# Kernel tuning notes

Hardware: AMD Instinct MI355X
Metric: run time of the kernel (lower is better)

Reference implementation:

```python
import jax, jax.numpy as jnp
import numpy as np

C = 256      # in_channels
NH = 4       # n_heads
NG = 32      # GroupNorm num_groups
EPS = 1e-5   # torch GroupNorm default eps


def _conv1x1(x, w, b):
    # 1x1 conv == per-pixel channel matmul. x: (B,C,H,W), w: (O,C), b: (O,)
    return jnp.einsum('oc,bchw->bohw', w, x) + b[None, :, None, None]


def _groupnorm(x, gamma, beta):
    b, c, h, w = x.shape
    xg = x.reshape(b, NG, c // NG, h, w)
    mu = xg.mean(axis=(2, 3, 4), keepdims=True)
    var = xg.var(axis=(2, 3, 4), keepdims=True)
    xn = ((xg - mu) * jax.lax.rsqrt(var + EPS)).reshape(b, c, h, w)
    return xn * gamma[None, :, None, None] + beta[None, :, None, None]


def setup_inputs() -> dict:
    key = jax.random.key(0)
    ks = jax.random.split(key, 5)
    B, H, W = 2, 64, 64
    s = 1.0 / np.sqrt(C).astype(np.float32)
    return {
        'x': jax.random.normal(ks[0], (B, C, H, W), jnp.float32),
        'gamma': jnp.ones((C,), jnp.float32),
        'beta': jnp.zeros((C,), jnp.float32),
        'wq': jax.random.normal(ks[1], (C, C), jnp.float32) * s,
        'bq': jnp.zeros((C,), jnp.float32),
        'wk': jax.random.normal(ks[2], (C, C), jnp.float32) * s,
        'bk': jnp.zeros((C,), jnp.float32),
        'wv': jax.random.normal(ks[3], (C, C), jnp.float32) * s,
        'bv': jnp.zeros((C,), jnp.float32),
        'wp': jax.random.normal(ks[4], (C, C), jnp.float32) * s,
        'bp': jnp.zeros((C,), jnp.float32),
    }


def reference(x, gamma, beta, wq, bq, wk, bk, wv, bv, wp, bp):
    b, c, h, w = x.shape
    c_ = c // NH  # head dim
    hn = _groupnorm(x, gamma, beta)
    # NOTE: original splits channels as (head_dim, n_heads) with head_dim leading
    q = _conv1x1(hn, wq, bq).reshape(b, c_, NH, h * w)
    k = _conv1x1(hn, wk, bk).reshape(b, c_, NH, h * w)
    v = _conv1x1(hn, wv, bv).reshape(b, c_, NH, h * w)
    scores = jnp.einsum('bcnq,bcnk->bqkn', q, k) * (c_ ** -0.5)  # (B,S,S,NH)
    attn = jax.nn.softmax(scores, axis=2)  # softmax over key axis
    out = jnp.einsum('bcnd,bqdn->bcnq', v, attn).reshape(b, c, h, w)
    return x + _conv1x1(out, wp, bp)
```

## Files before the change

### kernel.cpp

```cpp
#include <hip/hip_runtime.h>

#define CH 256
#define NHEAD 4
#define HD 64
#define SP 4096
#define NB 2
#define QSCALE 0.1803368801111204f

typedef __attribute__((ext_vector_type(8))) short bf16x8;
typedef __attribute__((ext_vector_type(4))) float f32x4;
typedef unsigned int u32;
typedef unsigned short u16;

__device__ inline u16 b16(float f) {
    u32 u = __float_as_uint(f);
    return (u16)((u + 0x8000u) >> 16);
}
__device__ inline float fexp2(float x) { return __builtin_amdgcn_exp2f(x); }

__global__ __launch_bounds__(256) void prep_kernel(
    const float* __restrict__ x, float2* __restrict__ part,
    const float* __restrict__ wq, const float* __restrict__ wk,
    const float* __restrict__ wv, const float* __restrict__ wp,
    u16* __restrict__ wqb, u16* __restrict__ wkb,
    u16* __restrict__ wvb, u16* __restrict__ wpb)
{
    int tid = threadIdx.x;
    if (blockIdx.x < 256) {
        int bgq = blockIdx.x;
        int bg = bgq >> 2, qtr = bgq & 3;
        const float4* xp = (const float4*)(x + (size_t)bg * 8 * SP) + qtr * 2048;
        float s = 0.f, ss = 0.f;
        for (int i = tid; i < 2048; i += 256) {
            float4 u = xp[i];
            s  += (u.x + u.y) + (u.z + u.w);
            ss += (u.x * u.x + u.y * u.y) + (u.z * u.z + u.w * u.w);
        }
#pragma unroll
        for (int off = 32; off > 0; off >>= 1) {
            s  += __shfl_down(s, off);
            ss += __shfl_down(ss, off);
        }
        __shared__ float ws_s[4], ws_q[4];
        int w = tid >> 6;
        if ((tid & 63) == 0) { ws_s[w] = s; ws_q[w] = ss; }
        __syncthreads();
        if (tid == 0)
            part[bgq] = make_float2(ws_s[0] + ws_s[1] + ws_s[2] + ws_s[3],
                                    ws_q[0] + ws_q[1] + ws_q[2] + ws_q[3]);
    } else {
        int idx = (blockIdx.x - 256) * 256 + tid;
        int m = idx >> 16, i = idx & 65535;
        if (m == 0)      wqb[i] = b16(wq[i] * QSCALE);
        else if (m == 1) wkb[i] = b16(wk[i]);
        else if (m == 2) wvb[i] = b16(wv[i]);
        else {
            int c = i >> 8, chan = i & 255;
            int n = chan >> 6, d = chan & 63;
            wpb[i] = b16(wp[c * 256 + d * 4 + n]);
        }
    }
}

__global__ __launch_bounds__(256) void qkv_gemm_kernel(
    const float* __restrict__ x, const float2* __restrict__ part,
    const float* __restrict__ gamma, const float* __restrict__ beta,
    const u16* __restrict__ wqb, const u16* __restrict__ wkb,
    const u16* __restrict__ wvb,
    const float* __restrict__ bq, const float* __restrict__ bk,
    const float* __restrict__ bv,
    u16* __restrict__ qt, u16* __restrict__ ktp, u16* __restrict__ vtp)
{
    int zz = blockIdx.y;
    int b = zz / 3, p = zz % 3;
    const u16* W = (p == 0) ? wqb : (p == 1) ? wkb : wvb;
    const float* bias = (p == 0) ? bq : (p == 1) ? bk : bv;
    float bs = (p == 0) ? QSCALE : 1.f;
    int s0 = blockIdx.x * 32;
    int tid = threadIdx.x, w = tid >> 6, lane = tid & 63;
    int t = lane >> 4, ln = lane & 15;

    __shared__ u16 SB[10240];
    __shared__ float As[256], Bs[256];

    {
        int c = tid, bg = b * 32 + (c >> 3);
        float s = 0.f, ss = 0.f;
#pragma unroll
        for (int q = 0; q < 4; q++) { float2 pp = part[bg * 4 + q]; s += pp.x; ss += pp.y; }
        float mu = s * (1.f / 32768.f);
        float var = ss * (1.f / 32768.f) - mu * mu;
        float rs = rsqrtf(var + 1e-5f);
        float ga = gamma[c];
        As[c] = rs * ga;
        Bs[c] = beta[c] - mu * rs * ga;
    }
    __syncthreads();

    {
        int cb = tid >> 3;
        int sseg = (tid & 7) * 4;
#pragma unroll
        for (int it = 0; it < 8; it++) {
            int c = it * 32 + cb;
            float4 v = *(const float4*)&x[((size_t)b * CH + c) * SP + s0 + sseg];
            float aa = As[c], bb = Bs[c];
            SB[(sseg + 0) * 264 + c] = b16(fmaf(aa, v.x, bb));
            SB[(sseg + 1) * 264 + c] = b16(fmaf(aa, v.y, bb));
            SB[(sseg + 2) * 264 + c] = b16(fmaf(aa, v.z, bb));
            SB[(sseg + 3) * 264 + c] = b16(fmaf(aa, v.w, bb));
        }
    }
    __syncthreads();

    f32x4 acc[4][2];
#pragma unroll
    for (int og = 0; og < 4; og++)
#pragma unroll
        for (int sg = 0; sg < 2; sg++)
            acc[og][sg] = (f32x4){0.f, 0.f, 0.f, 0.f};

#pragma unroll
    for (int ks = 0; ks < 8; ks++) {
        bf16x8 af[4], bfv[2];
#pragma unroll
        for (int og = 0; og < 4; og++)
            af[og] = *(const bf16x8*)&W[(size_t)(w * 64 + og * 16 + ln) * CH + ks * 32 + t * 8];
#pragma unroll
        for (int sg = 0; sg < 2; sg++)
            bfv[sg] = *(const bf16x8*)&SB[(sg * 16 + ln) * 264 + ks * 32 + t * 8];
#pragma unroll
        for (int og = 0; og < 4; og++)
#pragma unroll
            for (int sg = 0; sg < 2; sg++)
                acc[og][sg] = __builtin_amdgcn_mfma_f32_16x16x32_bf16(
                    af[og], bfv[sg], acc[og][sg], 0, 0, 0);
    }
    __syncthreads();

    if (p < 2) {
#pragma unroll
        for (int og = 0; og < 4; og++)
#pragma unroll
            for (int sg = 0; sg < 2; sg++)
#pragma unroll
                for (int r = 0; r < 4; r++) {
                    int o = w * 64 + og * 16 + 4 * t + r;
                    SB[(r * 32 + sg * 16 + ln) * 72 + (w * 16 + og * 4 + t)] =
                        b16(acc[og][sg][r] + bias[o] * bs);
                }
        __syncthreads();
        if (p == 0) {
#pragma unroll
            for (int it = 0; it < 4; it++) {
                int idx = it * 256 + tid;
                int o8 = idx & 7, sl = (idx >> 3) & 31, n = idx >> 8;
                *(uint4*)&qt[((size_t)(b * 4 + n) * SP + s0 + sl) * HD + o8 * 8] =
                    *(const uint4*)&SB[(n * 32 + sl) * 72 + o8 * 8];
            }
        } else {
#pragma unroll
            for (int it = 0; it < 4; it++) {
                int idx = it * 256 + tid;
                int o8 = idx & 7, sl = (idx >> 3) & 31, n = idx >> 8;
                int key = s0 + sl;
                int g = ((key >> 4) & 3) * 2 + (o8 >> 2);
                int lp = (key & 15) + 16 * (o8 & 3);
                *(uint4*)&ktp[(size_t)(b * 4 + n) * SP * HD +
                              (size_t)(key >> 6) * 4096 + g * 512 + lp * 8] =
                    *(const uint4*)&SB[(n * 32 + sl) * 72 + o8 * 8];
            }
        }
    } else {
#pragma unroll
        for (int og = 0; og < 4; og++)
#pragma unroll
            for (int sg = 0; sg < 2; sg++)
#pragma unroll
                for (int r = 0; r < 4; r++) {
                    int o = w * 64 + og * 16 + 4 * t + r;
                    SB[(r * 64 + w * 16 + og * 4 + t) * 40 + sg * 16 + ln] =
                        b16(acc[og][sg][r] + bias[o]);
                }
        __syncthreads();
#pragma unroll
        for (int it = 0; it < 4; it++) {
            int idx = it * 256 + tid;
            int so8 = idx & 3, d = (idx >> 2) & 63, n = idx >> 8;
            int key = s0 + so8 * 8;
            int g = ((d >> 4) & 3) * 2 + ((key >> 5) & 1);
            int lp = (d & 15) + 16 * ((key >> 3) & 3);
            *(uint4*)&vtp[(size_t)(b * 4 + n) * SP * HD +
                          (size_t)(key >> 6) * 4096 + g * 512 + lp * 8] =
                *(const uint4*)&SB[(n * 64 + d) * 40 + so8 * 8];
        }
    }
}

__global__ __launch_bounds__(256, 3) void attn_kernel(
    const u16* __restrict__ qtb, const u16* __restrict__ ktp,
    const u16* __restrict__ vtp, u16* __restrict__ opart,
    float* __restrict__ lpart)
{
    int bx = blockIdx.x;
    int z = bx & 7, qt_i = (bx >> 3) & 31, sp = bx >> 8;
    int sq0 = qt_i * 128;
    int tile0 = sp * 16;
    const u16* qz = qtb + (size_t)z * SP * HD;
    const u16* kz = ktp + (size_t)z * SP * HD;
    const u16* vz = vtp + (size_t)z * SP * HD;

    int tid = threadIdx.x, w = tid >> 6, l = tid & 63;
    int t = l >> 4, ln = l & 15;

    __shared__ __align__(16) u32 Pb[4][2][512];

    bf16x8 qf[2][2];
#pragma unroll
    for (int qg = 0; qg < 2; qg++)
#pragma unroll
        for (int ds = 0; ds < 2; ds++)
            qf[qg][ds] = *(const bf16x8*)&qz[
                (size_t)(sq0 + w * 32 + qg * 16 + ln) * HD + ds * 32 + t * 8];

    bf16x8 kf[8], vf[8];
#pragma unroll
    for (int g = 0; g < 8; g++)
        kf[g] = *(const bf16x8*)&kz[(size_t)tile0 * 4096 + g * 512 + l * 8];

    float lsum[2] = {0.f, 0.f};
    f32x4 oacc[2][4];
#pragma unroll
    for (int qg = 0; qg < 2; qg++)
#pragma unroll
        for (int dg = 0; dg < 4; dg++)
            oacc[qg][dg] = (f32x4){0.f, 0.f, 0.f, 0.f};

    const f32x4 z4 = {0.f, 0.f, 0.f, 0.f};
    f32x4 sa[2][4];

    auto ep = [&](int qg) {
#pragma unroll
        for (int kg = 0; kg < 4; kg++) {
            float e0 = fexp2(sa[qg][kg][0]);
            float e1 = fexp2(sa[qg][kg][1]);
            float e2 = fexp2(sa[qg][kg][2]);
            float e3 = fexp2(sa[qg][kg][3]);
            lsum[qg] += (e0 + e1) + (e2 + e3);
            u32 p0 = __builtin_amdgcn_perm(__float_as_uint(e1), __float_as_uint(e0), 0x07060302u);
            u32 p1 = __builtin_amdgcn_perm(__float_as_uint(e3), __float_as_uint(e2), 0x07060302u);
            int Lt = ln + 16 * (2 * (kg & 1) + (t >> 1));
            int ksg = kg >> 1;
            *(uint2*)&Pb[w][qg][(ksg * 64 + Lt) * 4 + 2 * (t & 1)] =
                make_uint2(p0, p1);
        }
    };

    for (int kti = 0; kti < 16; kti++) {
        size_t tb = (size_t)(tile0 + kti) * 4096;

#pragma unroll
        for (int g = 0; g < 8; g++)
            vf[g] = *(const bf16x8*)&vz[tb + g * 512 + l * 8];

#pragma unroll
        for (int kg = 0; kg < 4; kg++) {
#pragma unroll
            for (int qg = 0; qg < 2; qg++)
                sa[qg][kg] = __builtin_amdgcn_mfma_f32_16x16x32_bf16(
                    kf[kg * 2 + 0], qf[qg][0], z4, 0, 0, 0);
        }
#pragma unroll
        for (int kg = 0; kg < 4; kg++) {
#pragma unroll
            for (int qg = 0; qg < 2; qg++)
                sa[qg][kg] = __builtin_amdgcn_mfma_f32_16x16x32_bf16(
                    kf[kg * 2 + 1], qf[qg][1], sa[qg][kg], 0, 0, 0);
        }

        if (kti < 15) {
            size_t nb = tb + 4096;
#pragma unroll
            for (int g = 0; g < 8; g++)
                kf[g] = *(const bf16x8*)&kz[nb + g * 512 + l * 8];
        }

        ep(0);
#pragma unroll
        for (int qg = 0; qg < 2; qg++) {
            if (qg == 0) ep(1);
            bf16x8 pf[2];
#pragma unroll
            for (int ksg = 0; ksg < 2; ksg++)
                pf[ksg] = *(const bf16x8*)&Pb[w][qg][(ksg * 64 + l) * 4];
#pragma unroll
            for (int ksg = 0; ksg < 2; ksg++)
#pragma unroll
                for (int dg = 0; dg < 4; dg++)
                    oacc[qg][dg] = __builtin_amdgcn_mfma_f32_16x16x32_bf16(
                        pf[ksg], vf[dg * 2 + ksg], oacc[qg][dg], 0, 0, 0);
        }
    }

#pragma unroll
    for (int qg = 0; qg < 2; qg++) {
        lsum[qg] += __shfl_xor(lsum[qg], 16);
        lsum[qg] += __shfl_xor(lsum[qg], 32);
    }

    size_t obase = (size_t)(sp * 8 + z) * SP;
    u16* po = (u16*)&Pb[w][0][0];
#pragma unroll
    for (int qg = 0; qg < 2; qg++)
#pragma unroll
        for (int dg = 0; dg < 4; dg++)
#pragma unroll
            for (int r = 0; r < 4; r++)
                po[(qg * 16 + 4 * t + r) * 64 + dg * 16 + ln] = b16(oacc[qg][dg][r]);
#pragma unroll
    for (int i = 0; i < 4; i++) {
        int f = i * 512 + l * 8;
        int qloc = f >> 6, d0 = f & 63;
        uint4 v = *(const uint4*)&po[f];
        *(uint4*)&opart[(obase + sq0 + w * 32 + qloc) * HD + d0] = v;
    }
    if (t == 0)
#pragma unroll
        for (int qg = 0; qg < 2; qg++)
            lpart[obase + sq0 + w * 32 + qg * 16 + ln] = lsum[qg];
}

__global__ __launch_bounds__(256) void proj_gemm_kernel(
    const u16* __restrict__ opart, const float* __restrict__ lpart,
    const u16* __restrict__ wpb, const float* __restrict__ bp,
    const float* __restrict__ x, float* __restrict__ out)
{
    int b = blockIdx.y;
    int s0 = blockIdx.x * 16;
    int tid = threadIdx.x, w = tid >> 6, lane = tid & 63;
    int t = lane >> 4, ln = lane & 15;

    float linv[4];
#pragma unroll
    for (int n = 0; n < 4; n++) {
        float s = 0.f;
#pragma unroll
        for (int sp = 0; sp < 4; sp++)
            s += lpart[(size_t)(sp * 8 + b * 4 + n) * SP + s0 + ln];
        linv[n] = 1.f / s;
    }

    f32x4 acc[4];
#pragma unroll
    for (int og = 0; og < 4; og++)
        acc[og] = (f32x4){0.f, 0.f, 0.f, 0.f};

#pragma unroll
    for (int ks = 0; ks < 8; ks++) {
        bf16x8 af[4];
#pragma unroll
        for (int og = 0; og < 4; og++)
            af[og] = *(const bf16x8*)&wpb[(size_t)(w * 64 + og * 16 + ln) * CH + ks * 32 + t * 8];

        int n = ks >> 1;
        int d0 = (ks & 1) * 32 + t * 8;
        u32 ov[4][4];
#pragma unroll
        for (int sp = 0; sp < 4; sp++) {
            uint4 o4 = *(const uint4*)&opart[
                ((size_t)(sp * 8 + b * 4 + n) * SP + s0 + ln) * HD + d0];
            ov[sp][0] = o4.x; ov[sp][1] = o4.y; ov[sp][2] = o4.z; ov[sp][3] = o4.w;
        }
        float inv = linv[n];
        union { u32 u[4]; bf16x8 v; } bu;
#pragma unroll
        for (int i = 0; i < 4; i++) {
            float lo = 0.f, hi = 0.f;
#pragma unroll
            for (int sp = 0; sp < 4; sp++) {
                lo += __uint_as_float(ov[sp][i] << 16);
                hi += __uint_as_float(ov[sp][i] & 0xffff0000u);
            }
            u16 rl = b16(lo * inv), rh = b16(hi * inv);
            bu.u[i] = ((u32)rh << 16) | rl;
        }
#pragma unroll
        for (int og = 0; og < 4; og++)
            acc[og] = __builtin_amdgcn_mfma_f32_16x16x32_bf16(
                af[og], bu.v, acc[og], 0, 0, 0);
    }

#pragma unroll
    for (int og = 0; og < 4; og++)
#pragma unroll
        for (int r = 0; r < 4; r++) {
            int c = w * 64 + og * 16 + 4 * t + r;
            size_t idx = ((size_t)b * CH + c) * SP + s0 + ln;
            out[idx] = acc[og][r] + bp[c] + x[idx];
        }
}

extern "C" void kernel_launch(void* const* d_in, const int* in_sizes, int n_in,
                              void* d_out, int out_size, void* d_ws, size_t ws_size,
                              hipStream_t stream)
{
    const float* x     = (const float*)d_in[0];
    const float* gamma = (const float*)d_in[1];
    const float* beta  = (const float*)d_in[2];
    const float* wq = (const float*)d_in[3]; const float* bq = (const float*)d_in[4];
    const float* wk = (const float*)d_in[5]; const float* bk = (const float*)d_in[6];
    const float* wv = (const float*)d_in[7]; const float* bv = (const float*)d_in[8];
    const float* wp = (const float*)d_in[9]; const float* bp = (const float*)d_in[10];
    float* out = (float*)d_out;

    const size_t TEN = (size_t)8 * SP * HD;
    char* wsb = (char*)d_ws;
    float2* part = (float2*)wsb;
    u16* wqb = (u16*)(wsb + 4096);
    u16* wkb = wqb + 65536;
    u16* wvb = wkb + 65536;
    u16* wpb = wvb + 65536;
    u16* qt  = wpb + 65536;
    u16* ktp = qt + TEN;
    u16* vtp = ktp + TEN;
    u16* opart = vtp + TEN;
    float* lpart = (float*)(opart + 4 * TEN);

    prep_kernel<<<dim3(1280), dim3(256), 0, stream>>>(
        x, part, wq, wk, wv, wp, wqb, wkb, wvb, wpb);
    qkv_gemm_kernel<<<dim3(128, 6), dim3(256), 0, stream>>>(
        x, part, gamma, beta, wqb, wkb, wvb, bq, bk, bv, qt, ktp, vtp);
    attn_kernel<<<dim3(1024), dim3(256), 0, stream>>>(qt, ktp, vtp, opart, lpart);
    proj_gemm_kernel<<<dim3(256, 2), dim3(256), 0, stream>>>(
        opart, lpart, wpb, bp, x, out);
}
```

Measured before the change: 159.8 us.

## Increase split-KV parallelism, shrink QKV tiles, and stage merged attention output in LDS

The attention kernel now takes the KV split count as a runtime parameter and uses 8 splits when the workspace is large enough, otherwise 4. Launch bounds are raised to 5 waves per SIMD to favour occupancy. The QKV GEMM uses 16-pixel tiles, doubling its grid and cutting LDS use. The projection kernel merges the split partials once into a shared-memory tile instead of reloading them inside each k-step. More splits add partial-output traffic and merge work, and the higher occupancy target may force register spills in the attention kernel.

```diff
diff --git a/kernel.cpp b/kernel.cpp
--- a/kernel.cpp
+++ b/kernel.cpp
@@ -76,11 +76,11 @@
     const u16* W = (p == 0) ? wqb : (p == 1) ? wkb : wvb;
     const float* bias = (p == 0) ? bq : (p == 1) ? bk : bv;
     float bs = (p == 0) ? QSCALE : 1.f;
-    int s0 = blockIdx.x * 32;
+    int s0 = blockIdx.x * 16;
     int tid = threadIdx.x, w = tid >> 6, lane = tid & 63;
     int t = lane >> 4, ln = lane & 15;
 
-    __shared__ u16 SB[10240];
+    __shared__ u16 SB[6144];
     __shared__ float As[256], Bs[256];
 
     {
@@ -98,11 +98,10 @@
     __syncthreads();
 
     {
-        int cb = tid >> 3;
-        int sseg = (tid & 7) * 4;
-#pragma unroll
-        for (int it = 0; it < 8; it++) {
-            int c = it * 32 + cb;
+        int cb = tid >> 2, sseg = (tid & 3) * 4;
+#pragma unroll
+        for (int it = 0; it < 4; it++) {
+            int c = it * 64 + cb;
             float4 v = *(const float4*)&x[((size_t)b * CH + c) * SP + s0 + sseg];
             float aa = As[c], bb = Bs[c];
             SB[(sseg + 0) * 264 + c] = b16(fmaf(aa, v.x, bb));
@@ -113,28 +112,22 @@
     }
     __syncthreads();
 
-    f32x4 acc[4][2];
+    f32x4 acc[4];
 #pragma unroll
     for (int og = 0; og < 4; og++)
-#pragma unroll
-        for (int sg = 0; sg < 2; sg++)
-            acc[og][sg] = (f32x4){0.f, 0.f, 0.f, 0.f};
+        acc[og] = (f32x4){0.f, 0.f, 0.f, 0.f};
 
 #pragma unroll
     for (int ks = 0; ks < 8; ks++) {
-        bf16x8 af[4], bfv[2];
+        bf16x8 af[4];
 #pragma unroll
         for (int og = 0; og < 4; og++)
             af[og] = *(const bf16x8*)&W[(size_t)(w * 64 + og * 16 + ln) * CH + ks * 32 + t * 8];
-#pragma unroll
-        for (int sg = 0; sg < 2; sg++)
-            bfv[sg] = *(const bf16x8*)&SB[(sg * 16 + ln) * 264 + ks * 32 + t * 8];
-#pragma unroll
-        for (int og = 0; og < 4; og++)
-#pragma unroll
-            for (int sg = 0; sg < 2; sg++)
-                acc[og][sg] = __builtin_amdgcn_mfma_f32_16x16x32_bf16(
-                    af[og], bfv[sg], acc[og][sg], 0, 0, 0);
+        bf16x8 bfv = *(const bf16x8*)&SB[ln * 264 + ks * 32 + t * 8];
+#pragma unroll
+        for (int og = 0; og < 4; og++)
+            acc[og] = __builtin_amdgcn_mfma_f32_16x16x32_bf16(
+                af[og], bfv, acc[og], 0, 0, 0);
     }
     __syncthreads();
 
@@ -142,70 +135,66 @@
 #pragma unroll
         for (int og = 0; og < 4; og++)
 #pragma unroll
-            for (int sg = 0; sg < 2; sg++)
-#pragma unroll
-                for (int r = 0; r < 4; r++) {
-                    int o = w * 64 + og * 16 + 4 * t + r;
-                    SB[(r * 32 + sg * 16 + ln) * 72 + (w * 16 + og * 4 + t)] =
-                        b16(acc[og][sg][r] + bias[o] * bs);
-                }
+            for (int r = 0; r < 4; r++) {
+                int o = w * 64 + og * 16 + 4 * t + r;
+                SB[(r * 16 + ln) * 72 + (w * 16 + og * 4 + t)] =
+                    b16(acc[og][r] + bias[o] * bs);
+            }
         __syncthreads();
         if (p == 0) {
 #pragma unroll
-            for (int it = 0; it < 4; it++) {
-                int idx = it * 256 + tid;
-                int o8 = idx & 7, sl = (idx >> 3) & 31, n = idx >> 8;
+            for (int it = 0; it < 2; it++) {
+                int f = it * 256 + tid;
+                int o8 = f & 7, sl = (f >> 3) & 15, n = f >> 7;
                 *(uint4*)&qt[((size_t)(b * 4 + n) * SP + s0 + sl) * HD + o8 * 8] =
-                    *(const uint4*)&SB[(n * 32 + sl) * 72 + o8 * 8];
+                    *(const uint4*)&SB[(n * 16 + sl) * 72 + o8 * 8];
             }
         } else {
 #pragma unroll
-            for (int it = 0; it < 4; it++) {
-                int idx = it * 256 + tid;
-                int o8 = idx & 7, sl = (idx >> 3) & 31, n = idx >> 8;
+            for (int it = 0; it < 2; it++) {
+                int f = it * 256 + tid;
+                int o8 = f & 7, sl = (f >> 3) & 15, n = f >> 7;
                 int key = s0 + sl;
                 int g = ((key >> 4) & 3) * 2 + (o8 >> 2);
                 int lp = (key & 15) + 16 * (o8 & 3);
                 *(uint4*)&ktp[(size_t)(b * 4 + n) * SP * HD +
                               (size_t)(key >> 6) * 4096 + g * 512 + lp * 8] =
-                    *(const uint4*)&SB[(n * 32 + sl) * 72 + o8 * 8];
+                    *(const uint4*)&SB[(n * 16 + sl) * 72 + o8 * 8];
             }
         }
     } else {
 #pragma unroll
         for (int og = 0; og < 4; og++)
 #pragma unroll
-            for (int sg = 0; sg < 2; sg++)
-#pragma unroll
-                for (int r = 0; r < 4; r++) {
-                    int o = w * 64 + og * 16 + 4 * t + r;
-                    SB[(r * 64 + w * 16 + og * 4 + t) * 40 + sg * 16 + ln] =
-                        b16(acc[og][sg][r] + bias[o]);
-                }
+            for (int r = 0; r < 4; r++) {
+                int o = w * 64 + og * 16 + 4 * t + r;
+                SB[(r * 64 + w * 16 + og * 4 + t) * 24 + ln] =
+                    b16(acc[og][r] + bias[o]);
+            }
         __syncthreads();
 #pragma unroll
-        for (int it = 0; it < 4; it++) {
-            int idx = it * 256 + tid;
-            int so8 = idx & 3, d = (idx >> 2) & 63, n = idx >> 8;
+        for (int it = 0; it < 2; it++) {
+            int f = it * 256 + tid;
+            int so8 = f & 1, d = (f >> 1) & 63, n = f >> 7;
             int key = s0 + so8 * 8;
             int g = ((d >> 4) & 3) * 2 + ((key >> 5) & 1);
             int lp = (d & 15) + 16 * ((key >> 3) & 3);
             *(uint4*)&vtp[(size_t)(b * 4 + n) * SP * HD +
                           (size_t)(key >> 6) * 4096 + g * 512 + lp * 8] =
-                *(const uint4*)&SB[(n * 64 + d) * 40 + so8 * 8];
-        }
-    }
-}
-
-__global__ __launch_bounds__(256, 3) void attn_kernel(
+                *(const uint4*)&SB[(n * 64 + d) * 24 + so8 * 8];
+        }
+    }
+}
+
+__global__ __launch_bounds__(256, 5) void attn_kernel(
     const u16* __restrict__ qtb, const u16* __restrict__ ktp,
     const u16* __restrict__ vtp, u16* __restrict__ opart,
-    float* __restrict__ lpart)
+    float* __restrict__ lpart, int nt)
 {
     int bx = blockIdx.x;
     int z = bx & 7, qt_i = (bx >> 3) & 31, sp = bx >> 8;
     int sq0 = qt_i * 128;
-    int tile0 = sp * 16;
+    int tile0 = sp * nt;
     const u16* qz = qtb + (size_t)z * SP * HD;
     const u16* kz = ktp + (size_t)z * SP * HD;
     const u16* vz = vtp + (size_t)z * SP * HD;
@@ -256,7 +245,7 @@
         }
     };
 
-    for (int kti = 0; kti < 16; kti++) {
+    for (int kti = 0; kti < nt; kti++) {
         size_t tb = (size_t)(tile0 + kti) * 4096;
 
 #pragma unroll
@@ -264,21 +253,19 @@
             vf[g] = *(const bf16x8*)&vz[tb + g * 512 + l * 8];
 
 #pragma unroll
-        for (int kg = 0; kg < 4; kg++) {
+        for (int kg = 0; kg < 4; kg++)
 #pragma unroll
             for (int qg = 0; qg < 2; qg++)
                 sa[qg][kg] = __builtin_amdgcn_mfma_f32_16x16x32_bf16(
                     kf[kg * 2 + 0], qf[qg][0], z4, 0, 0, 0);
-        }
-#pragma unroll
-        for (int kg = 0; kg < 4; kg++) {
+#pragma unroll
+        for (int kg = 0; kg < 4; kg++)
 #pragma unroll
             for (int qg = 0; qg < 2; qg++)
                 sa[qg][kg] = __builtin_amdgcn_mfma_f32_16x16x32_bf16(
                     kf[kg * 2 + 1], qf[qg][1], sa[qg][kg], 0, 0, 0);
-        }
-
-        if (kti < 15) {
+
+        if (kti < nt - 1) {
             size_t nb = tb + 4096;
 #pragma unroll
             for (int g = 0; g < 8; g++)
@@ -333,22 +320,44 @@
 __global__ __launch_bounds__(256) void proj_gemm_kernel(
     const u16* __restrict__ opart, const float* __restrict__ lpart,
     const u16* __restrict__ wpb, const float* __restrict__ bp,
-    const float* __restrict__ x, float* __restrict__ out)
+    const float* __restrict__ x, float* __restrict__ out, int nsplit)
 {
     int b = blockIdx.y;
     int s0 = blockIdx.x * 16;
     int tid = threadIdx.x, w = tid >> 6, lane = tid & 63;
     int t = lane >> 4, ln = lane & 15;
 
-    float linv[4];
-#pragma unroll
-    for (int n = 0; n < 4; n++) {
-        float s = 0.f;
-#pragma unroll
-        for (int sp = 0; sp < 4; sp++)
-            s += lpart[(size_t)(sp * 8 + b * 4 + n) * SP + s0 + ln];
-        linv[n] = 1.f / s;
-    }
+    __shared__ u16 BsL[16 * 264];
+
+#pragma unroll
+    for (int it = 0; it < 2; it++) {
+        int f = it * 256 + tid;
+        int oct = f & 31, s = f >> 5;
+        int n = oct >> 3, d0 = (oct & 7) * 8;
+        float lsumv = 0.f;
+        float accv[8] = {0.f,0.f,0.f,0.f,0.f,0.f,0.f,0.f};
+        for (int sp = 0; sp < nsplit; sp++) {
+            size_t base = (size_t)(sp * 8 + b * 4 + n) * SP + s0 + s;
+            lsumv += lpart[base];
+            uint4 o4 = *(const uint4*)&opart[base * HD + d0];
+            u32 ov[4] = {o4.x, o4.y, o4.z, o4.w};
+#pragma unroll
+            for (int i = 0; i < 4; i++) {
+                accv[2 * i + 0] += __uint_as_float(ov[i] << 16);
+                accv[2 * i + 1] += __uint_as_float(ov[i] & 0xffff0000u);
+            }
+        }
+        float inv = 1.f / lsumv;
+        u32 res[4];
+#pragma unroll
+        for (int i = 0; i < 4; i++) {
+            u16 rl = b16(accv[2 * i + 0] * inv);
+            u16 rh = b16(accv[2 * i + 1] * inv);
+            res[i] = ((u32)rh << 16) | rl;
+        }
+        *(uint4*)&BsL[s * 264 + oct * 8] = make_uint4(res[0], res[1], res[2], res[3]);
+    }
+    __syncthreads();
 
     f32x4 acc[4];
 #pragma unroll
@@ -361,33 +370,11 @@
 #pragma unroll
         for (int og = 0; og < 4; og++)
             af[og] = *(const bf16x8*)&wpb[(size_t)(w * 64 + og * 16 + ln) * CH + ks * 32 + t * 8];
-
-        int n = ks >> 1;
-        int d0 = (ks & 1) * 32 + t * 8;
-        u32 ov[4][4];
-#pragma unroll
-        for (int sp = 0; sp < 4; sp++) {
-            uint4 o4 = *(const uint4*)&opart[
-                ((size_t)(sp * 8 + b * 4 + n) * SP + s0 + ln) * HD + d0];
-            ov[sp][0] = o4.x; ov[sp][1] = o4.y; ov[sp][2] = o4.z; ov[sp][3] = o4.w;
-        }
-        float inv = linv[n];
-        union { u32 u[4]; bf16x8 v; } bu;
-#pragma unroll
-        for (int i = 0; i < 4; i++) {
-            float lo = 0.f, hi = 0.f;
-#pragma unroll
-            for (int sp = 0; sp < 4; sp++) {
-                lo += __uint_as_float(ov[sp][i] << 16);
-                hi += __uint_as_float(ov[sp][i] & 0xffff0000u);
-            }
-            u16 rl = b16(lo * inv), rh = b16(hi * inv);
-            bu.u[i] = ((u32)rh << 16) | rl;
-        }
+        bf16x8 bfv = *(const bf16x8*)&BsL[ln * 264 + ks * 32 + t * 8];
 #pragma unroll
         for (int og = 0; og < 4; og++)
             acc[og] = __builtin_amdgcn_mfma_f32_16x16x32_bf16(
-                af[og], bu.v, acc[og], 0, 0, 0);
+                af[og], bfv, acc[og], 0, 0, 0);
     }
 
 #pragma unroll
@@ -414,6 +401,10 @@
     float* out = (float*)d_out;
 
     const size_t TEN = (size_t)8 * SP * HD;
+    const size_t NEED8 = 4096 + 524288 + 3 * TEN * 2 + 8 * TEN * 2 + 8 * 8 * SP * 4;
+    int nsplit = (ws_size >= NEED8) ? 8 : 4;
+    int nt = 64 / nsplit;
+
     char* wsb = (char*)d_ws;
     float2* part = (float2*)wsb;
     u16* wqb = (u16*)(wsb + 4096);
@@ -424,13 +415,14 @@
     u16* ktp = qt + TEN;
     u16* vtp = ktp + TEN;
     u16* opart = vtp + TEN;
-    float* lpart = (float*)(opart + 4 * TEN);
+    float* lpart = (float*)(opart + (size_t)nsplit * TEN);
 
     prep_kernel<<<dim3(1280), dim3(256), 0, stream>>>(
         x, part, wq, wk, wv, wp, wqb, wkb, wvb, wpb);
-    qkv_gemm_kernel<<<dim3(128, 6), dim3(256), 0, stream>>>(
+    qkv_gemm_kernel<<<dim3(256, 6), dim3(256), 0, stream>>>(
         x, part, gamma, beta, wqb, wkb, wvb, bq, bk, bv, qt, ktp, vtp);
-    attn_kernel<<<dim3(1024), dim3(256), 0, stream>>>(qt, ktp, vtp, opart, lpart);
+    attn_kernel<<<dim3(256 * nsplit), dim3(256), 0, stream>>>(
+        qt, ktp, vtp, opart, lpart, nt);
     proj_gemm_kernel<<<dim3(256, 2), dim3(256), 0, stream>>>(
-        opart, lpart, wpb, bp, x, out);
-}
+        opart, lpart, wpb, bp, x, out, nsplit);
+}
```

After: 474.3 us. 197% more time.
